# Performance work log

Hardware: AMD Instinct MI355X
Metric: run time of the kernel (lower is better)

## Reference

```python
import jax, jax.numpy as jnp
import numpy as np

N_NODES = 100000


def _sage_conv(x, src, dst, W_l, b_l, W_r):
    # mean-aggregate neighbor (source) features at target nodes
    gathered = x[src]                                   # [E, D]
    summed = jax.ops.segment_sum(gathered, dst, num_segments=N_NODES)  # [N, D]
    deg = jax.ops.segment_sum(jnp.ones((src.shape[0],), x.dtype), dst,
                              num_segments=N_NODES)     # [N]
    mean = summed / jnp.maximum(deg, 1.0)[:, None]      # zero stays zero for isolated nodes
    # PyG SAGEConv: lin_l(aggr) + lin_r(x); bias on lin_l only
    return mean @ W_l + b_l + x @ W_r


def setup_inputs() -> dict:
    key = jax.random.key(0)
    ks = jax.random.split(key, 9)
    x = jax.random.normal(ks[0], (N_NODES, 128), dtype=jnp.float32)
    edge_index = jax.random.randint(ks[1], (2, 1600000), 0, N_NODES, dtype=jnp.int64)
    s1 = 1.0 / np.sqrt(128.0)
    s2 = 1.0 / np.sqrt(32.0)
    return {
        "x": x,
        "edge_index": edge_index,
        "W1_l": jax.random.normal(ks[2], (128, 32), jnp.float32) * s1,
        "b1_l": jax.random.normal(ks[3], (32,), jnp.float32) * s1,
        "W1_r": jax.random.normal(ks[4], (128, 32), jnp.float32) * s1,
        "W2_l": jax.random.normal(ks[5], (32, 32), jnp.float32) * s2,
        "b2_l": jax.random.normal(ks[6], (32,), jnp.float32) * s2,
        "W2_r": jax.random.normal(ks[7], (32, 32), jnp.float32) * s2,
    }


def reference(x, edge_index, W1_l, b1_l, W1_r, W2_l, b2_l, W2_r):
    src, dst = edge_index[0], edge_index[1]
    h = _sage_conv(x, src, dst, W1_l, b1_l, W1_r)
    h = jax.nn.relu(h)
    # dropout is identity in eval mode
    h = _sage_conv(h, src, dst, W2_l, b2_l, W2_r)
    return jax.nn.relu(h)
```

## Files before the change

kernel.cpp:

```cpp
#include <hip/hip_runtime.h>


typedef _Float16 f16;
typedef _Float16 f16x2 __attribute__((ext_vector_type(2)));
typedef _Float16 f16x4 __attribute__((ext_vector_type(4)));
typedef _Float16 half8 __attribute__((ext_vector_type(8)));
typedef float f32x4 __attribute__((ext_vector_type(4)));

#define MAXBINS 2048
#define SHIFT 6
#define BINSZ 64
#define CAP 48
#define BSTR 52
#define GSC 256
#define BSC 512
#define SRC_BITS 17
#define SRC_MASK 0x1FFFFu
#define XSTRIDE 136


__global__ __launch_bounds__(256) void gemm_mfma(const float* __restrict__ x,
                                                 const float* __restrict__ Wl,
                                                 const float* __restrict__ Wr,
                                                 f16* __restrict__ yl,
                                                 float* __restrict__ yr,
                                                 int N) {
    __shared__ __align__(16) f16 sX[64 * XSTRIDE];
    __shared__ __align__(16) f16 sWT[64 * XSTRIDE];
    const int tid = threadIdx.x;
    const int row0 = blockIdx.x * 64;

    for (int i = tid; i < 64 * 32; i += 256) {
        int r = i >> 5, c4 = i & 31;
        int row = row0 + r;
        float4 v = make_float4(0.f, 0.f, 0.f, 0.f);
        if (row < N) v = *(const float4*)(x + (size_t)row * 128 + c4 * 4);
        f16* d = &sX[r * XSTRIDE + c4 * 4];
        d[0] = (f16)v.x; d[1] = (f16)v.y; d[2] = (f16)v.z; d[3] = (f16)v.w;
    }
    for (int i = tid; i < 64 * 128; i += 256) {
        int k = i >> 6, n = i & 63;
        float v = (n < 32) ? Wl[k * 32 + n] : Wr[k * 32 + (n - 32)];
        sWT[n * XSTRIDE + k] = (f16)v;
    }
    __syncthreads();

    const int w = tid >> 6;
    const int lane = tid & 63;
    const int l15 = lane & 15, quad = lane >> 4;
    f32x4 acc[4] = {};
#pragma unroll
    for (int kc = 0; kc < 4; ++kc) {
        half8 af = *(const half8*)&sX[(w * 16 + l15) * XSTRIDE + kc * 32 + quad * 8];
#pragma unroll
        for (int nt = 0; nt < 4; ++nt) {
            half8 bf = *(const half8*)&sWT[(nt * 16 + l15) * XSTRIDE + kc * 32 + quad * 8];
            acc[nt] = __builtin_amdgcn_mfma_f32_16x16x32_f16(af, bf, acc[nt], 0, 0, 0);
        }
    }
#pragma unroll
    for (int nt = 0; nt < 4; ++nt) {
        int c = nt * 16 + l15;
#pragma unroll
        for (int r = 0; r < 4; ++r) {
            int g = row0 + w * 16 + quad * 4 + r;
            if (c < 32) yl[(size_t)g * 32 + c] = (f16)acc[nt][r];
            else        yr[(size_t)g * 32 + (c - 32)] = acc[nt][r];
        }
    }
}


__global__ __launch_bounds__(BSC) void scatter_sort(const int* __restrict__ src,
                                                    const int* __restrict__ dst,
                                                    unsigned* __restrict__ pairs,
                                                    unsigned* __restrict__ binSeg,
                                                    int E, int chunk) {
    __shared__ int cnt[MAXBINS];
    __shared__ int wsum[8];
    const int tid = threadIdx.x;
    const int sb = blockIdx.x;
    for (int i = tid; i < MAXBINS; i += BSC) cnt[i] = 0;
    __syncthreads();

    const int base = sb * chunk;
    const int endE = base + chunk < E ? base + chunk : E;
    const int len = endE > base ? endE - base : 0;
    const int nv = len >> 2;
    const int rem = len & 3;
    const int4* s4 = (const int4*)(src + base);
    const int4* d4 = (const int4*)(dst + base);

    for (int i = tid; i < nv; i += BSC) {
        int4 d = d4[i];
        atomicAdd(&cnt[d.x >> SHIFT], 1);
        atomicAdd(&cnt[d.y >> SHIFT], 1);
        atomicAdd(&cnt[d.z >> SHIFT], 1);
        atomicAdd(&cnt[d.w >> SHIFT], 1);
    }
    if (tid < rem) atomicAdd(&cnt[dst[base + nv * 4 + tid] >> SHIFT], 1);
    __syncthreads();

    {
        int b0 = cnt[4 * tid], b1 = cnt[4 * tid + 1],
            b2 = cnt[4 * tid + 2], b3 = cnt[4 * tid + 3];
        int tsum = b0 + b1 + b2 + b3;
        const int lane = tid & 63, wave = tid >> 6;
        int incl = tsum;
#pragma unroll
        for (int off = 1; off < 64; off <<= 1) {
            int t = __shfl_up(incl, off, 64);
            if (lane >= off) incl += t;
        }
        if (lane == 63) wsum[wave] = incl;
        __syncthreads();
        if (tid == 0) {
            int a = 0;
#pragma unroll
            for (int w = 0; w < 8; ++w) { int t = wsum[w]; wsum[w] = a; a += t; }
        }
        __syncthreads();
        int ex = (incl - tsum) + wsum[wave];
        int e0 = ex, e1 = ex + b0, e2 = e1 + b1, e3 = e2 + b2;
        binSeg[(size_t)(4 * tid) * GSC + sb]     = ((unsigned)e0 << 16) | (unsigned)b0;
        binSeg[(size_t)(4 * tid + 1) * GSC + sb] = ((unsigned)e1 << 16) | (unsigned)b1;
        binSeg[(size_t)(4 * tid + 2) * GSC + sb] = ((unsigned)e2 << 16) | (unsigned)b2;
        binSeg[(size_t)(4 * tid + 3) * GSC + sb] = ((unsigned)e3 << 16) | (unsigned)b3;
        __syncthreads();
        cnt[4 * tid] = e0; cnt[4 * tid + 1] = e1;
        cnt[4 * tid + 2] = e2; cnt[4 * tid + 3] = e3;
    }
    __syncthreads();

    unsigned* out = pairs + (size_t)sb * chunk;
    for (int i = tid; i < nv; i += BSC) {
        int4 s = s4[i];
        int4 d = d4[i];
        int slot;
        slot = atomicAdd(&cnt[d.x >> SHIFT], 1);
        out[slot] = ((unsigned)(d.x & (BINSZ - 1)) << SRC_BITS) | (unsigned)s.x;
        slot = atomicAdd(&cnt[d.y >> SHIFT], 1);
        out[slot] = ((unsigned)(d.y & (BINSZ - 1)) << SRC_BITS) | (unsigned)s.y;
        slot = atomicAdd(&cnt[d.z >> SHIFT], 1);
        out[slot] = ((unsigned)(d.z & (BINSZ - 1)) << SRC_BITS) | (unsigned)s.z;
        slot = atomicAdd(&cnt[d.w >> SHIFT], 1);
        out[slot] = ((unsigned)(d.w & (BINSZ - 1)) << SRC_BITS) | (unsigned)s.w;
    }
    if (tid < rem) {
        int e = base + nv * 4 + tid;
        int s = src[e], d = dst[e];
        int slot = atomicAdd(&cnt[d >> SHIFT], 1);
        out[slot] = ((unsigned)(d & (BINSZ - 1)) << SRC_BITS) | (unsigned)s;
    }
}


__device__ __forceinline__ void build_bucket(const unsigned* __restrict__ pairs,
                                             const unsigned* __restrict__ binSeg,
                                             int* sBucket, int* sCnt,
                                             int b, int tid, int chunk) {
    unsigned dsc = binSeg[(size_t)b * GSC + tid];
    int scnt = (int)(dsc & 0xFFFFu);
    const unsigned* p = pairs + (size_t)tid * chunk + (dsc >> 16);
    int k = 0;
    for (; k + 4 <= scnt; k += 4) {
        unsigned p0 = p[k], p1 = p[k + 1], p2 = p[k + 2], p3 = p[k + 3];
        int l, s;
        l = p0 >> SRC_BITS; s = atomicAdd(&sCnt[l], 1);
        if (s < CAP) sBucket[l * BSTR + s] = (int)(p0 & SRC_MASK);
        l = p1 >> SRC_BITS; s = atomicAdd(&sCnt[l], 1);
        if (s < CAP) sBucket[l * BSTR + s] = (int)(p1 & SRC_MASK);
        l = p2 >> SRC_BITS; s = atomicAdd(&sCnt[l], 1);
        if (s < CAP) sBucket[l * BSTR + s] = (int)(p2 & SRC_MASK);
        l = p3 >> SRC_BITS; s = atomicAdd(&sCnt[l], 1);
        if (s < CAP) sBucket[l * BSTR + s] = (int)(p3 & SRC_MASK);
    }
    for (; k < scnt; ++k) {
        unsigned pk = p[k];
        int l = pk >> SRC_BITS;
        int s = atomicAdd(&sCnt[l], 1);
        if (s < CAP) sBucket[l * BSTR + s] = (int)(pk & SRC_MASK);
    }
}

__global__ __launch_bounds__(256) void agg_l1(const unsigned* __restrict__ pairs,
                                              const unsigned* __restrict__ binSeg,
                                              const f16* __restrict__ yl,
                                              const float* __restrict__ yr,
                                              const float* __restrict__ b1,
                                              const float* __restrict__ W2l,
                                              const float* __restrict__ W2r,
                                              f16* __restrict__ zl,
                                              float* __restrict__ zr,
                                              int N, int chunk) {
    __shared__ __align__(16) int sBucket[BINSZ * BSTR];
    __shared__ int sCnt[BINSZ];
    __shared__ __align__(16) float sW[2048];
    __shared__ __align__(16) float sB[32];
    const int tid = threadIdx.x;
    if (tid < BINSZ) sCnt[tid] = 0;
    if (tid < 32) sB[tid] = b1[tid];
    {
        float4* sW4 = (float4*)sW;
        sW4[tid] = ((const float4*)W2l)[tid];
        sW4[256 + tid] = ((const float4*)W2r)[tid];
        for (int i = tid; i < BINSZ * BSTR; i += 256) sBucket[i] = N;
    }
    __syncthreads();

    const int b = blockIdx.x;
    build_bucket(pairs, binSeg, sBucket, sCnt, b, tid, chunk);
    __syncthreads();

    const int node = tid >> 2;
    const int c8 = tid & 3;
    const int node0 = b << SHIFT;
    const int g = node0 + node;

    const int deg = sCnt[node];
    const int m = deg < CAP ? deg : CAP;
    const int q = (m + 7) >> 3;
    const int4* bk = (const int4*)&sBucket[node * BSTR];
    const f16* yb = yl + c8 * 8;

    float ax[8] = {0.f, 0.f, 0.f, 0.f, 0.f, 0.f, 0.f, 0.f};
    for (int j = 0; j < q; ++j) {
        int4 eA = bk[2 * j];
        int4 eB = bk[2 * j + 1];
        half8 v0 = *(const half8*)(yb + (size_t)eA.x * 32);
        half8 v1 = *(const half8*)(yb + (size_t)eA.y * 32);
        half8 v2 = *(const half8*)(yb + (size_t)eA.z * 32);
        half8 v3 = *(const half8*)(yb + (size_t)eA.w * 32);
        half8 w0 = *(const half8*)(yb + (size_t)eB.x * 32);
        half8 w1 = *(const half8*)(yb + (size_t)eB.y * 32);
        half8 w2 = *(const half8*)(yb + (size_t)eB.z * 32);
        half8 w3 = *(const half8*)(yb + (size_t)eB.w * 32);
#pragma unroll
        for (int k = 0; k < 8; ++k)
            ax[k] += (((float)v0[k] + (float)v1[k]) + ((float)v2[k] + (float)v3[k]))
                   + (((float)w0[k] + (float)w1[k]) + ((float)w2[k] + (float)w3[k]));
    }

    float h[8];
    if (g < N) {
        float dg = deg > 1 ? (float)deg : 1.0f;
        float loc[8];
        *(float4*)&loc[0] = *(const float4*)(yr + (size_t)g * 32 + c8 * 8);
        *(float4*)&loc[4] = *(const float4*)(yr + (size_t)g * 32 + c8 * 8 + 4);
#pragma unroll
        for (int k = 0; k < 8; ++k)
            h[k] = fmaxf(ax[k] / dg + sB[c8 * 8 + k] + loc[k], 0.0f);
    } else {
#pragma unroll
        for (int k = 0; k < 8; ++k) h[k] = 0.f;
    }
    __syncthreads();

    float* sH = (float*)sBucket;
    *(float4*)&sH[node * 36 + c8 * 8]     = make_float4(h[0], h[1], h[2], h[3]);
    *(float4*)&sH[node * 36 + c8 * 8 + 4] = make_float4(h[4], h[5], h[6], h[7]);
    __syncthreads();

    const int n2 = tid >> 3;
    const int cq = tid & 7;
    const float4* sW4l = (const float4*)sW;
    const float4* sW4r = (const float4*)(sW + 1024);
#pragma unroll
    for (int it = 0; it < 2; ++it) {
        int n = it * 32 + n2;
        int gg = node0 + n;
        float4 al = make_float4(0.f, 0.f, 0.f, 0.f);
        float4 ar = make_float4(0.f, 0.f, 0.f, 0.f);
#pragma unroll 8
        for (int k = 0; k < 32; ++k) {
            float hk = sH[n * 36 + k];
            float4 wl = sW4l[k * 8 + cq];
            float4 wr = sW4r[k * 8 + cq];
            al.x += hk * wl.x; al.y += hk * wl.y; al.z += hk * wl.z; al.w += hk * wl.w;
            ar.x += hk * wr.x; ar.y += hk * wr.y; ar.z += hk * wr.z; ar.w += hk * wr.w;
        }
        f16x4 hh;
        hh[0] = (f16)al.x; hh[1] = (f16)al.y; hh[2] = (f16)al.z; hh[3] = (f16)al.w;
        *(f16x4*)(zl + (size_t)gg * 32 + cq * 4) = hh;
        if (gg < N) *(float4*)(zr + (size_t)gg * 32 + cq * 4) = ar;
    }
}

__global__ __launch_bounds__(256) void agg_l2(const unsigned* __restrict__ pairs,
                                              const unsigned* __restrict__ binSeg,
                                              const f16* __restrict__ zl,
                                              const float* __restrict__ b2,
                                              float* __restrict__ io,
                                              int N, int chunk) {
    __shared__ __align__(16) int sBucket[BINSZ * BSTR];
    __shared__ int sCnt[BINSZ];
    __shared__ __align__(16) float sB[32];
    const int tid = threadIdx.x;
    if (tid < BINSZ) sCnt[tid] = 0;
    if (tid < 32) sB[tid] = b2[tid];
    for (int i = tid; i < BINSZ * BSTR; i += 256) sBucket[i] = N;
    __syncthreads();

    const int b = blockIdx.x;
    build_bucket(pairs, binSeg, sBucket, sCnt, b, tid, chunk);
    __syncthreads();

    const int node = tid >> 2;
    const int c8 = tid & 3;
    const int node0 = b << SHIFT;
    const int g = node0 + node;

    const int deg = sCnt[node];
    const int m = deg < CAP ? deg : CAP;
    const int q = (m + 7) >> 3;
    const int4* bk = (const int4*)&sBucket[node * BSTR];
    const f16* zb = zl + c8 * 8;

    float ax[8] = {0.f, 0.f, 0.f, 0.f, 0.f, 0.f, 0.f, 0.f};
    for (int j = 0; j < q; ++j) {
        int4 eA = bk[2 * j];
        int4 eB = bk[2 * j + 1];
        half8 v0 = *(const half8*)(zb + (size_t)eA.x * 32);
        half8 v1 = *(const half8*)(zb + (size_t)eA.y * 32);
        half8 v2 = *(const half8*)(zb + (size_t)eA.z * 32);
        half8 v3 = *(const half8*)(zb + (size_t)eA.w * 32);
        half8 w0 = *(const half8*)(zb + (size_t)eB.x * 32);
        half8 w1 = *(const half8*)(zb + (size_t)eB.y * 32);
        half8 w2 = *(const half8*)(zb + (size_t)eB.z * 32);
        half8 w3 = *(const half8*)(zb + (size_t)eB.w * 32);
#pragma unroll
        for (int k = 0; k < 8; ++k)
            ax[k] += (((float)v0[k] + (float)v1[k]) + ((float)v2[k] + (float)v3[k]))
                   + (((float)w0[k] + (float)w1[k]) + ((float)w2[k] + (float)w3[k]));
    }

    if (g < N) {
        float dg = deg > 1 ? (float)deg : 1.0f;
        float v[8];
        *(float4*)&v[0] = *(const float4*)(io + (size_t)g * 32 + c8 * 8);
        *(float4*)&v[4] = *(const float4*)(io + (size_t)g * 32 + c8 * 8 + 4);
        float o[8];
#pragma unroll
        for (int k = 0; k < 8; ++k)
            o[k] = fmaxf(ax[k] / dg + sB[c8 * 8 + k] + v[k], 0.0f);
        *(float4*)(io + (size_t)g * 32 + c8 * 8)     = *(float4*)&o[0];
        *(float4*)(io + (size_t)g * 32 + c8 * 8 + 4) = *(float4*)&o[4];
    }
}

extern "C" void kernel_launch(void* const* d_in, const int* in_sizes, int n_in,
                              void* d_out, int out_size, void* d_ws, size_t ws_size,
                              hipStream_t stream) {
    const float* x    = (const float*)d_in[0];
    const int*   ei   = (const int*)d_in[1];
    const float* W1l  = (const float*)d_in[2];
    const float* b1l  = (const float*)d_in[3];
    const float* W1r  = (const float*)d_in[4];
    const float* W2l  = (const float*)d_in[5];
    const float* b2l  = (const float*)d_in[6];
    const float* W2r  = (const float*)d_in[7];

    const int N = in_sizes[0] / 128;
    const int E = in_sizes[1] / 2;
    const int* srcIdx = ei;
    const int* dstIdx = ei + E;

    const int gridG = (N >> 6) + 1;
    const int NP = gridG << 6;

    const int nbins = (N + BINSZ - 1) >> SHIFT;
    const int chunk = (((E + GSC - 1) / GSC) + 3) & ~3;

    unsigned* binSeg = (unsigned*)d_ws;
    unsigned* pairs  = binSeg + (size_t)MAXBINS * GSC;
    f16*      A      = (f16*)(pairs + (size_t)GSC * chunk);
    float*    B      = (float*)(A + (size_t)NP * 32);
    f16*      Z      = (f16*)(B + (size_t)NP * 32);
    float*    outp   = (float*)d_out;

    gemm_mfma<<<gridG, 256, 0, stream>>>(x, W1l, W1r, A, B, N);
    scatter_sort<<<GSC, BSC, 0, stream>>>(srcIdx, dstIdx, pairs, binSeg, E, chunk);
    agg_l1<<<nbins, 256, 0, stream>>>(pairs, binSeg, A, B, b1l,
                                      W2l, W2r, Z, outp, N, chunk);
    agg_l2<<<nbins, 256, 0, stream>>>(pairs, binSeg, Z, b2l, outp, N, chunk);
}
```

Baseline: 194.8 us.

## Double aggregation threads per bin with split edge loops and shuffle reduction

Both aggregation kernels now launch 512 threads per 64-node bin instead of 256. Pairs of threads split each node's neighbour list and combine partial sums with a lane shuffle. Bucket building is also split across two threads per source segment, and the per-node residual loads are hoisted ahead of the gather loop. The aim is more memory-level parallelism and occupancy for the latency-bound random gathers, at the cost of extra shuffles and a launch-bounds constraint that may raise register pressure.

Result: slower. 209.8 us (+7.7%).

```diff
diff --git a/kernel.cpp b/kernel.cpp
--- a/kernel.cpp
+++ b/kernel.cpp
@@ -159,23 +159,12 @@
                                              const unsigned* __restrict__ binSeg,
                                              int* sBucket, int* sCnt,
                                              int b, int tid, int chunk) {
-    unsigned dsc = binSeg[(size_t)b * GSC + tid];
+    unsigned dsc = binSeg[(size_t)b * GSC + (tid >> 1)];
     int scnt = (int)(dsc & 0xFFFFu);
-    const unsigned* p = pairs + (size_t)tid * chunk + (dsc >> 16);
-    int k = 0;
-    for (; k + 4 <= scnt; k += 4) {
-        unsigned p0 = p[k], p1 = p[k + 1], p2 = p[k + 2], p3 = p[k + 3];
-        int l, s;
-        l = p0 >> SRC_BITS; s = atomicAdd(&sCnt[l], 1);
-        if (s < CAP) sBucket[l * BSTR + s] = (int)(p0 & SRC_MASK);
-        l = p1 >> SRC_BITS; s = atomicAdd(&sCnt[l], 1);
-        if (s < CAP) sBucket[l * BSTR + s] = (int)(p1 & SRC_MASK);
-        l = p2 >> SRC_BITS; s = atomicAdd(&sCnt[l], 1);
-        if (s < CAP) sBucket[l * BSTR + s] = (int)(p2 & SRC_MASK);
-        l = p3 >> SRC_BITS; s = atomicAdd(&sCnt[l], 1);
-        if (s < CAP) sBucket[l * BSTR + s] = (int)(p3 & SRC_MASK);
-    }
-    for (; k < scnt; ++k) {
+    const unsigned* p = pairs + (size_t)(tid >> 1) * chunk + (dsc >> 16);
+    const int k0 = (tid & 1) ? (scnt >> 1) : 0;
+    const int k1 = (tid & 1) ? scnt : (scnt >> 1);
+    for (int k = k0; k < k1; ++k) {
         unsigned pk = p[k];
         int l = pk >> SRC_BITS;
         int s = atomicAdd(&sCnt[l], 1);
@@ -183,16 +172,16 @@
     }
 }
 
-__global__ __launch_bounds__(256) void agg_l1(const unsigned* __restrict__ pairs,
-                                              const unsigned* __restrict__ binSeg,
-                                              const f16* __restrict__ yl,
-                                              const float* __restrict__ yr,
-                                              const float* __restrict__ b1,
-                                              const float* __restrict__ W2l,
-                                              const float* __restrict__ W2r,
-                                              f16* __restrict__ zl,
-                                              float* __restrict__ zr,
-                                              int N, int chunk) {
+__global__ __launch_bounds__(512, 8) void agg_l1(const unsigned* __restrict__ pairs,
+                                                 const unsigned* __restrict__ binSeg,
+                                                 const f16* __restrict__ yl,
+                                                 const float* __restrict__ yr,
+                                                 const float* __restrict__ b1,
+                                                 const float* __restrict__ W2l,
+                                                 const float* __restrict__ W2r,
+                                                 f16* __restrict__ zl,
+                                                 float* __restrict__ zr,
+                                                 int N, int chunk) {
     __shared__ __align__(16) int sBucket[BINSZ * BSTR];
     __shared__ int sCnt[BINSZ];
     __shared__ __align__(16) float sW[2048];
@@ -200,22 +189,23 @@
     const int tid = threadIdx.x;
     if (tid < BINSZ) sCnt[tid] = 0;
     if (tid < 32) sB[tid] = b1[tid];
-    {
-        float4* sW4 = (float4*)sW;
-        sW4[tid] = ((const float4*)W2l)[tid];
-        sW4[256 + tid] = ((const float4*)W2r)[tid];
-        for (int i = tid; i < BINSZ * BSTR; i += 256) sBucket[i] = N;
-    }
+    ((float4*)sW)[tid] = (tid < 256) ? ((const float4*)W2l)[tid]
+                                     : ((const float4*)W2r)[tid - 256];
+    for (int i = tid; i < BINSZ * BSTR; i += 512) sBucket[i] = N;
     __syncthreads();
 
     const int b = blockIdx.x;
     build_bucket(pairs, binSeg, sBucket, sCnt, b, tid, chunk);
     __syncthreads();
 
-    const int node = tid >> 2;
-    const int c8 = tid & 3;
+    const int node = tid >> 3;
+    const int c8 = (tid >> 1) & 3;
+    const int eh = tid & 1;
     const int node0 = b << SHIFT;
     const int g = node0 + node;
+
+    float4 locA = *(const float4*)(yr + (size_t)g * 32 + c8 * 8);
+    float4 locB = *(const float4*)(yr + (size_t)g * 32 + c8 * 8 + 4);
 
     const int deg = sCnt[node];
     const int m = deg < CAP ? deg : CAP;
@@ -224,7 +214,7 @@
     const f16* yb = yl + c8 * 8;
 
     float ax[8] = {0.f, 0.f, 0.f, 0.f, 0.f, 0.f, 0.f, 0.f};
-    for (int j = 0; j < q; ++j) {
+    for (int j = eh; j < q; j += 2) {
         int4 eA = bk[2 * j];
         int4 eB = bk[2 * j + 1];
         half8 v0 = *(const half8*)(yb + (size_t)eA.x * 32);
@@ -240,13 +230,15 @@
             ax[k] += (((float)v0[k] + (float)v1[k]) + ((float)v2[k] + (float)v3[k]))
                    + (((float)w0[k] + (float)w1[k]) + ((float)w2[k] + (float)w3[k]));
     }
+#pragma unroll
+    for (int k = 0; k < 8; ++k) ax[k] += __shfl_xor(ax[k], 1, 64);
 
     float h[8];
     if (g < N) {
         float dg = deg > 1 ? (float)deg : 1.0f;
         float loc[8];
-        *(float4*)&loc[0] = *(const float4*)(yr + (size_t)g * 32 + c8 * 8);
-        *(float4*)&loc[4] = *(const float4*)(yr + (size_t)g * 32 + c8 * 8 + 4);
+        *(float4*)&loc[0] = locA;
+        *(float4*)&loc[4] = locB;
 #pragma unroll
         for (int k = 0; k < 8; ++k)
             h[k] = fmaxf(ax[k] / dg + sB[c8 * 8 + k] + loc[k], 0.0f);
@@ -257,58 +249,64 @@
     __syncthreads();
 
     float* sH = (float*)sBucket;
-    *(float4*)&sH[node * 36 + c8 * 8]     = make_float4(h[0], h[1], h[2], h[3]);
-    *(float4*)&sH[node * 36 + c8 * 8 + 4] = make_float4(h[4], h[5], h[6], h[7]);
+    if (eh == 0)
+        *(float4*)&sH[node * 36 + c8 * 8]     = make_float4(h[0], h[1], h[2], h[3]);
+    else
+        *(float4*)&sH[node * 36 + c8 * 8 + 4] = make_float4(h[4], h[5], h[6], h[7]);
     __syncthreads();
 
     const int n2 = tid >> 3;
     const int cq = tid & 7;
     const float4* sW4l = (const float4*)sW;
     const float4* sW4r = (const float4*)(sW + 1024);
-#pragma unroll
-    for (int it = 0; it < 2; ++it) {
-        int n = it * 32 + n2;
-        int gg = node0 + n;
-        float4 al = make_float4(0.f, 0.f, 0.f, 0.f);
-        float4 ar = make_float4(0.f, 0.f, 0.f, 0.f);
+    int gg = node0 + n2;
+    float4 al = make_float4(0.f, 0.f, 0.f, 0.f);
+    float4 ar = make_float4(0.f, 0.f, 0.f, 0.f);
 #pragma unroll 8
-        for (int k = 0; k < 32; ++k) {
-            float hk = sH[n * 36 + k];
-            float4 wl = sW4l[k * 8 + cq];
-            float4 wr = sW4r[k * 8 + cq];
-            al.x += hk * wl.x; al.y += hk * wl.y; al.z += hk * wl.z; al.w += hk * wl.w;
-            ar.x += hk * wr.x; ar.y += hk * wr.y; ar.z += hk * wr.z; ar.w += hk * wr.w;
-        }
-        f16x4 hh;
-        hh[0] = (f16)al.x; hh[1] = (f16)al.y; hh[2] = (f16)al.z; hh[3] = (f16)al.w;
-        *(f16x4*)(zl + (size_t)gg * 32 + cq * 4) = hh;
-        if (gg < N) *(float4*)(zr + (size_t)gg * 32 + cq * 4) = ar;
-    }
-}
-
-__global__ __launch_bounds__(256) void agg_l2(const unsigned* __restrict__ pairs,
-                                              const unsigned* __restrict__ binSeg,
-                                              const f16* __restrict__ zl,
-                                              const float* __restrict__ b2,
-                                              float* __restrict__ io,
-                                              int N, int chunk) {
+    for (int k = 0; k < 32; ++k) {
+        float hk = sH[n2 * 36 + k];
+        float4 wl = sW4l[k * 8 + cq];
+        float4 wr = sW4r[k * 8 + cq];
+        al.x += hk * wl.x; al.y += hk * wl.y; al.z += hk * wl.z; al.w += hk * wl.w;
+        ar.x += hk * wr.x; ar.y += hk * wr.y; ar.z += hk * wr.z; ar.w += hk * wr.w;
+    }
+    f16x4 hh;
+    hh[0] = (f16)al.x; hh[1] = (f16)al.y; hh[2] = (f16)al.z; hh[3] = (f16)al.w;
+    *(f16x4*)(zl + (size_t)gg * 32 + cq * 4) = hh;
+    if (gg < N) *(float4*)(zr + (size_t)gg * 32 + cq * 4) = ar;
+}
+
+__global__ __launch_bounds__(512, 8) void agg_l2(const unsigned* __restrict__ pairs,
+                                                 const unsigned* __restrict__ binSeg,
+                                                 const f16* __restrict__ zl,
+                                                 const float* __restrict__ b2,
+                                                 float* __restrict__ io,
+                                                 int N, int chunk) {
     __shared__ __align__(16) int sBucket[BINSZ * BSTR];
     __shared__ int sCnt[BINSZ];
     __shared__ __align__(16) float sB[32];
     const int tid = threadIdx.x;
     if (tid < BINSZ) sCnt[tid] = 0;
     if (tid < 32) sB[tid] = b2[tid];
-    for (int i = tid; i < BINSZ * BSTR; i += 256) sBucket[i] = N;
+    for (int i = tid; i < BINSZ * BSTR; i += 512) sBucket[i] = N;
     __syncthreads();
 
     const int b = blockIdx.x;
     build_bucket(pairs, binSeg, sBucket, sCnt, b, tid, chunk);
     __syncthreads();
 
-    const int node = tid >> 2;
-    const int c8 = tid & 3;
+    const int node = tid >> 3;
+    const int c8 = (tid >> 1) & 3;
+    const int eh = tid & 1;
     const int node0 = b << SHIFT;
     const int g = node0 + node;
+
+    float4 ioA = make_float4(0.f, 0.f, 0.f, 0.f);
+    float4 ioB = make_float4(0.f, 0.f, 0.f, 0.f);
+    if (g < N) {
+        ioA = *(const float4*)(io + (size_t)g * 32 + c8 * 8);
+        ioB = *(const float4*)(io + (size_t)g * 32 + c8 * 8 + 4);
+    }
 
     const int deg = sCnt[node];
     const int m = deg < CAP ? deg : CAP;
@@ -317,7 +315,7 @@
     const f16* zb = zl + c8 * 8;
 
     float ax[8] = {0.f, 0.f, 0.f, 0.f, 0.f, 0.f, 0.f, 0.f};
-    for (int j = 0; j < q; ++j) {
+    for (int j = eh; j < q; j += 2) {
         int4 eA = bk[2 * j];
         int4 eB = bk[2 * j + 1];
         half8 v0 = *(const half8*)(zb + (size_t)eA.x * 32);
@@ -333,18 +331,22 @@
             ax[k] += (((float)v0[k] + (float)v1[k]) + ((float)v2[k] + (float)v3[k]))
                    + (((float)w0[k] + (float)w1[k]) + ((float)w2[k] + (float)w3[k]));
     }
+#pragma unroll
+    for (int k = 0; k < 8; ++k) ax[k] += __shfl_xor(ax[k], 1, 64);
 
     if (g < N) {
         float dg = deg > 1 ? (float)deg : 1.0f;
         float v[8];
-        *(float4*)&v[0] = *(const float4*)(io + (size_t)g * 32 + c8 * 8);
-        *(float4*)&v[4] = *(const float4*)(io + (size_t)g * 32 + c8 * 8 + 4);
+        *(float4*)&v[0] = ioA;
+        *(float4*)&v[4] = ioB;
         float o[8];
 #pragma unroll
         for (int k = 0; k < 8; ++k)
             o[k] = fmaxf(ax[k] / dg + sB[c8 * 8 + k] + v[k], 0.0f);
-        *(float4*)(io + (size_t)g * 32 + c8 * 8)     = *(float4*)&o[0];
-        *(float4*)(io + (size_t)g * 32 + c8 * 8 + 4) = *(float4*)&o[4];
+        if (eh == 0)
+            *(float4*)(io + (size_t)g * 32 + c8 * 8)     = *(float4*)&o[0];
+        else
+            *(float4*)(io + (size_t)g * 32 + c8 * 8 + 4) = *(float4*)&o[4];
     }
 }
 
@@ -380,7 +382,7 @@
 
     gemm_mfma<<<gridG, 256, 0, stream>>>(x, W1l, W1r, A, B, N);
     scatter_sort<<<GSC, BSC, 0, stream>>>(srcIdx, dstIdx, pairs, binSeg, E, chunk);
-    agg_l1<<<nbins, 256, 0, stream>>>(pairs, binSeg, A, B, b1l,
+    agg_l1<<<nbins, 512, 0, stream>>>(pairs, binSeg, A, B, b1l,
                                       W2l, W2r, Z, outp, N, chunk);
-    agg_l2<<<nbins, 256, 0, stream>>>(pairs, binSeg, Z, b2l, outp, N, chunk);
-}
+    agg_l2<<<nbins, 512, 0, stream>>>(pairs, binSeg, Z, b2l, outp, N, chunk);
+}
```
